# Optimization experiments

Hardware: AMD Instinct MI355X
Metric: run time of the kernel (lower is better)

Reference implementation:

```python
import jax, jax.numpy as jnp
import numpy as np

B, S, I, H = 256, 512, 512, 1024


def setup_inputs() -> dict:
    key = jax.random.key(0)
    ks = jax.random.split(key, 7)
    s = 1.0 / np.sqrt(H)
    x = jax.random.normal(ks[0], (B, S, I), jnp.float32)
    # equinox GRUCell params: weight_ih (3H,I), weight_hh (3H,H), bias (3H,), bias_n (H,)
    wi = jax.random.uniform(ks[1], (3 * H, I), jnp.float32, -s, s)
    wh = jax.random.uniform(ks[2], (3 * H, H), jnp.float32, -s, s)
    bi = jax.random.uniform(ks[3], (3 * H,), jnp.float32, -s, s)
    bn = jax.random.uniform(ks[4], (H,), jnp.float32, -s, s)
    # final Linear(H, 1)
    sl = 1.0 / np.sqrt(H)
    wl = jax.random.uniform(ks[5], (1, H), jnp.float32, -sl, sl)
    bl = jax.random.uniform(ks[6], (1,), jnp.float32, -sl, sl)
    return {"x": x, "wi": wi, "wh": wh, "bi": bi, "bn": bn, "wl": wl, "bl": bl}


def reference(x, wi, wh, bi, bn, wl, bl):
    # x: (B, S, I). Precompute input-side gate projections for all timesteps
    # (same math as per-step wi @ x_t + bi, hoisted out of the scan).
    ig_all = jnp.einsum('bsi,gi->sbg', x, wi) + bi  # (S, B, 3H)

    def step(h, ig_t):
        hg = h @ wh.T  # (B, 3H)
        ir, iz, ia = jnp.split(ig_t, 3, axis=-1)
        hr, hz, ha = jnp.split(hg, 3, axis=-1)
        r = jax.nn.sigmoid(ir + hr)          # reset gate
        z = jax.nn.sigmoid(iz + hz)          # update gate (equinox 'inp')
        n = jnp.tanh(ia + r * (ha + bn))     # candidate (uses bias_n)
        h_new = n + z * (h - n)              # equinox GRUCell output
        return h_new, None

    h0 = jnp.zeros((x.shape[0], wh.shape[1]), x.dtype)
    hT, _ = jax.lax.scan(step, h0, ig_all)
    energies = hT @ wl.T + bl  # (B, 1)
    return jnp.squeeze(energies, axis=-1)  # (B,)
```

## Files before the change

### kernel.cpp

```cpp
#include <hip/hip_runtime.h>
#include <hip/hip_bf16.h>


#define B_  256
#define S_  512
#define I_  512
#define H_  1024

typedef __bf16 bf16x8 __attribute__((ext_vector_type(8)));
typedef float  f32x4  __attribute__((ext_vector_type(4)));
typedef float  f32x4v __attribute__((ext_vector_type(4)));

union U16x8 { int4 i; bf16x8 b; unsigned short s[8]; unsigned u[4]; };

__device__ __forceinline__ unsigned pack2bf(float lo, float hi) {
    union { float f; unsigned u; } a, b;
    a.f = lo; b.f = hi;
    return __builtin_amdgcn_perm(b.u + 0x8000u, a.u + 0x8000u, 0x07060302u);
}
__device__ __forceinline__ bf16x8 ldb(const unsigned short* p) {
    U16x8 u; u.i = *(const int4*)p; return u.b;
}
__device__ __forceinline__ bf16x8 ldh_dev(const unsigned long long* p) {
    unsigned long long lo = __hip_atomic_load(p,     __ATOMIC_RELAXED, __HIP_MEMORY_SCOPE_AGENT);
    unsigned long long hi = __hip_atomic_load(p + 1, __ATOMIC_RELAXED, __HIP_MEMORY_SCOPE_AGENT);
    union { unsigned long long q[2]; bf16x8 b; } u;
    u.q[0] = lo; u.q[1] = hi; return u.b;
}

__global__ void prep_kernel(const float* __restrict__ wh, const float* __restrict__ wi,
                            const float* __restrict__ x,
                            unsigned* __restrict__ hbA_u, unsigned* __restrict__ whb_u,
                            unsigned* __restrict__ wib_u, unsigned* __restrict__ flags,
                            unsigned* __restrict__ xb_u, unsigned* __restrict__ xw_u,
                            int W) {
    int idx = blockIdx.x * blockDim.x + threadIdx.x;
    int stride = gridDim.x * blockDim.x;
    const float2* wh2 = (const float2*)wh;
    const float2* wi2 = (const float2*)wi;
    for (int i = idx; i < 3 * H_ * H_ / 2; i += stride) { float2 v = wh2[i]; whb_u[i] = pack2bf(v.x, v.y); }
    for (int i = idx; i < 3 * H_ * I_ / 2; i += stride) { float2 v = wi2[i]; wib_u[i] = pack2bf(v.x, v.y); }
    for (int i = idx; i < B_ * H_ / 2; i += stride) hbA_u[i] = 0u;
    if (idx < 256 * 4 * 16) flags[idx] = 0u;
    if (xb_u) {
        const float2* x2 = (const float2*)x;
        const int n = B_ * S_ * I_ / 2;
        for (int i = idx; i < n; i += stride) { float2 v = x2[i]; xb_u[i] = pack2bf(v.x, v.y); }
    }
    if (xw_u) {
        const int total = 4 * W * 16384;
        for (int i = idx; i < total; i += stride) {
            int gslot = i >> 14;
            int rest  = i & 16383;
            int row   = rest >> 8;
            int cp    = rest & 255;
            int mt    = gslot / W;
            int s     = gslot - mt * W;
            const float2 v = *(const float2*)(x + ((size_t)(mt * 64 + row) * S_ + s) * I_ + (cp << 1));
            xw_u[i] = pack2bf(v.x, v.y);
        }
    }
}

template<int MODE>
__global__ __launch_bounds__(256, 1) void gru_persistent(
    const float* __restrict__ x,
    const unsigned short* __restrict__ xbp,
    unsigned* __restrict__ xww,
    const unsigned short* __restrict__ whb,
    const unsigned short* __restrict__ wib,
    const float* __restrict__ bi,
    const float* __restrict__ bn,
    unsigned short* __restrict__ hbufA,
    unsigned short* __restrict__ hbufB,
    float* __restrict__ h32g,
    unsigned* __restrict__ flags,
    int wmask)
{
    __shared__ float partial[4 * 3 * 16 * 68];
    __shared__ float h32s[64 * 17];

    const int tid  = threadIdx.x;
    const int w    = tid >> 6;
    const int lane = tid & 63;
    const int col  = lane & 15;
    const int quad = lane >> 4;

    const int hblk = blockIdx.x & 63;
    const int mt   = blockIdx.x >> 6;
    const int k0   = hblk << 4;
    const int b0   = mt << 6;
    const int kwh  = w << 8;
    const int kwi  = w << 7;

    bf16x8 Bh[3][8];
    bf16x8 Bx[3][4];
    #pragma unroll
    for (int g = 0; g < 3; ++g) {
        const unsigned short* bh = whb + ((size_t)(g * H_ + k0 + col)) * H_ + kwh + (quad << 3);
        #pragma unroll
        for (int kk = 0; kk < 8; ++kk) Bh[g][kk] = ldb(bh + kk * 32);
        const unsigned short* bx = wib + ((size_t)(g * H_ + k0 + col)) * I_ + kwi + (quad << 3);
        #pragma unroll
        for (int kk = 0; kk < 4; ++kk) Bx[g][kk] = ldb(bx + kk * 32);
    }

    const int hcol = k0 + col;
    const float bir = bi[hcol], biz = bi[H_ + hcol], bia = bi[2 * H_ + hcol], bnv = bn[hcol];

    for (int i = tid; i < 64 * 17; i += 256) h32s[i] = 0.f;
    __syncthreads();

    unsigned* myflag = flags + (((blockIdx.x << 2) + w) << 4);
    const unsigned* spin_fp = flags +
        ((((mt << 6) + (w << 4) + (lane >> 2)) * 4 + (lane & 3)) << 4);

    const f32x4 zero4 = {0.f, 0.f, 0.f, 0.f};

    for (int t = 0; t < S_; ++t) {
        f32x4 acc[4][4];
        #pragma unroll
        for (int mi = 0; mi < 4; ++mi)
            #pragma unroll
            for (int j = 0; j < 4; ++j) acc[mi][j] = zero4;

        bool early_ok = true;
        if (t > 0)
            early_ok = (__hip_atomic_load(spin_fp, __ATOMIC_RELAXED, __HIP_MEMORY_SCOPE_AGENT) >= (unsigned)t);

        if constexpr (MODE == 2) {
            const unsigned short* xbase = xbp + ((size_t)(b0 + col) * S_ + (size_t)t) * I_ + kwi + (quad << 3);
            #pragma unroll
            for (int kk = 0; kk < 4; ++kk) {
                #pragma unroll
                for (int mi = 0; mi < 4; ++mi) {
                    bf16x8 a = ldb(xbase + (size_t)mi * 16 * S_ * I_ + kk * 32);
                    acc[mi][0] = __builtin_amdgcn_mfma_f32_16x16x32_bf16(a, Bx[0][kk], acc[mi][0], 0, 0, 0);
                    acc[mi][1] = __builtin_amdgcn_mfma_f32_16x16x32_bf16(a, Bx[1][kk], acc[mi][1], 0, 0, 0);
                    acc[mi][2] = __builtin_amdgcn_mfma_f32_16x16x32_bf16(a, Bx[2][kk], acc[mi][2], 0, 0, 0);
                }
            }
        } else if constexpr (MODE == 1) {
            const int W = wmask + 1;
            const unsigned short* xbase = xbp
                + ((size_t)((mt * W + (t & wmask)) * 64 + col)) * I_ + kwi + (quad << 3);
            #pragma unroll
            for (int kk = 0; kk < 4; ++kk) {
                #pragma unroll
                for (int mi = 0; mi < 4; ++mi) {
                    bf16x8 a = ldh_dev((const unsigned long long*)(xbase + (size_t)mi * 16 * I_ + kk * 32));
                    acc[mi][0] = __builtin_amdgcn_mfma_f32_16x16x32_bf16(a, Bx[0][kk], acc[mi][0], 0, 0, 0);
                    acc[mi][1] = __builtin_amdgcn_mfma_f32_16x16x32_bf16(a, Bx[1][kk], acc[mi][1], 0, 0, 0);
                    acc[mi][2] = __builtin_amdgcn_mfma_f32_16x16x32_bf16(a, Bx[2][kk], acc[mi][2], 0, 0, 0);
                }
            }
        } else {
            const float* xbase = x + ((size_t)(b0 + col) * S_ + (size_t)t) * I_ + kwi + (quad << 3);
            #pragma unroll
            for (int kk = 0; kk < 4; ++kk) {
                #pragma unroll
                for (int mi = 0; mi < 4; ++mi) {
                    const float* p = xbase + (size_t)mi * 16 * S_ * I_ + kk * 32;
                    f32x4v f0 = __builtin_nontemporal_load((const f32x4v*)p);
                    f32x4v f1 = __builtin_nontemporal_load((const f32x4v*)(p + 4));
                    U16x8 u;
                    u.u[0] = pack2bf(f0[0], f0[1]);
                    u.u[1] = pack2bf(f0[2], f0[3]);
                    u.u[2] = pack2bf(f1[0], f1[1]);
                    u.u[3] = pack2bf(f1[2], f1[3]);
                    bf16x8 a = u.b;
                    acc[mi][0] = __builtin_amdgcn_mfma_f32_16x16x32_bf16(a, Bx[0][kk], acc[mi][0], 0, 0, 0);
                    acc[mi][1] = __builtin_amdgcn_mfma_f32_16x16x32_bf16(a, Bx[1][kk], acc[mi][1], 0, 0, 0);
                    acc[mi][2] = __builtin_amdgcn_mfma_f32_16x16x32_bf16(a, Bx[2][kk], acc[mi][2], 0, 0, 0);
                }
            }
        }

        if (t > 0) {
            if (!early_ok) {
                while (__hip_atomic_load(spin_fp, __ATOMIC_RELAXED, __HIP_MEMORY_SCOPE_AGENT) < (unsigned)t)
                    __builtin_amdgcn_s_sleep(1);
            }
            asm volatile("" ::: "memory");
        }

        const unsigned short* hcur = (t & 1) ? hbufB : hbufA;
        const unsigned short* hrow = hcur + (size_t)(b0 + col) * H_ + kwh + (quad << 3);
        {
            bf16x8 hf[2][4];
            #pragma unroll
            for (int mi = 0; mi < 4; ++mi)
                hf[0][mi] = ldh_dev((const unsigned long long*)(hrow + (size_t)mi * 16 * H_));
            #pragma unroll
            for (int kk = 0; kk < 8; ++kk) {
                if (kk < 7) {
                    #pragma unroll
                    for (int mi = 0; mi < 4; ++mi)
                        hf[(kk + 1) & 1][mi] = ldh_dev((const unsigned long long*)(hrow + (size_t)mi * 16 * H_ + (kk + 1) * 32));
                }
                #pragma unroll
                for (int mi = 0; mi < 4; ++mi) {
                    bf16x8 a = hf[kk & 1][mi];
                    acc[mi][0] = __builtin_amdgcn_mfma_f32_16x16x32_bf16(a, Bh[0][kk], acc[mi][0], 0, 0, 0);
                    acc[mi][1] = __builtin_amdgcn_mfma_f32_16x16x32_bf16(a, Bh[1][kk], acc[mi][1], 0, 0, 0);
                    acc[mi][3] = __builtin_amdgcn_mfma_f32_16x16x32_bf16(a, Bh[2][kk], acc[mi][3], 0, 0, 0);
                }
            }
        }

        if constexpr (MODE == 1) {
            const int W = wmask + 1;
            const int s = t + W - 1;
            if (t >= 1 && s < S_) {
                const int flat = (hblk << 8) + tid;
                const int row  = flat >> 8;
                const int cp   = flat & 255;
                const float2 v = *(const float2*)(x + ((size_t)(b0 + row) * S_ + s) * I_ + (cp << 1));
                const unsigned pkt = pack2bf(v.x, v.y);
                __hip_atomic_store(xww + ((size_t)((mt * W + (s & wmask))) << 14) + flat,
                                   pkt, __ATOMIC_RELAXED, __HIP_MEMORY_SCOPE_AGENT);
            }
        }

        #pragma unroll
        for (int mi = 0; mi < 4; ++mi) {
            if (mi == w) continue;
            int slot = mi - (mi > w ? 1 : 0);
            float* dst = partial + (size_t)((w * 3 + slot) * 16) * 68;
            #pragma unroll
            for (int j = 0; j < 4; ++j)
                #pragma unroll
                for (int r = 0; r < 4; ++r)
                    dst[((quad << 2) + r) * 68 + j * 16 + col] = acc[mi][j][r];
        }
        __syncthreads();

        #pragma unroll
        for (int r = 0; r < 4; ++r) {
            float sr = 0.f, sz = 0.f, sia = 0.f, sha = 0.f;
            #pragma unroll
            for (int mi = 0; mi < 4; ++mi)
                if (mi == w) { sr = acc[mi][0][r]; sz = acc[mi][1][r]; sia = acc[mi][2][r]; sha = acc[mi][3][r]; }
            #pragma unroll
            for (int p = 0; p < 4; ++p) {
                if (p == w) continue;
                int slot = w - (w > p ? 1 : 0);
                const float* src = partial + (size_t)(((p * 3 + slot) * 16 + (quad << 2) + r)) * 68 + col;
                sr  += src[0];
                sz  += src[16];
                sia += src[32];
                sha += src[48];
            }
            float rg = 1.f / (1.f + __expf(-(sr + bir)));
            float zg = 1.f / (1.f + __expf(-(sz + biz)));
            float pa = sia + bia + rg * (sha + bnv);
            float e2 = __expf(2.f * pa);
            float ng = 1.f - 2.f / (e2 + 1.f);
            int m = (w << 4) + (quad << 2) + r;
            float hold = h32s[m * 17 + col];
            float hnew = ng + zg * (hold - ng);
            h32s[m * 17 + col] = hnew;
            if (t == S_ - 1) h32g[(size_t)(b0 + m) * H_ + k0 + col] = hnew;
        }
        __syncthreads();

        {
            unsigned short* hnext = (t & 1) ? hbufA : hbufB;
            const int pm = (w << 4) + (lane >> 2);
            const int pc = (lane & 3) << 2;
            const float* hp = h32s + pm * 17 + pc;
            unsigned long long pkt = (unsigned long long)pack2bf(hp[0], hp[1])
                                   | ((unsigned long long)pack2bf(hp[2], hp[3]) << 32);
            __hip_atomic_store((unsigned long long*)(hnext + (size_t)(b0 + pm) * H_ + k0 + pc),
                               pkt, __ATOMIC_RELAXED, __HIP_MEMORY_SCOPE_AGENT);
            asm volatile("s_waitcnt vmcnt(0)" ::: "memory");
            if (lane == 0)
                __hip_atomic_store(myflag, (unsigned)(t + 1), __ATOMIC_RELAXED, __HIP_MEMORY_SCOPE_AGENT);
        }
    }
}

__global__ __launch_bounds__(256) void final_kernel(const float* __restrict__ h32,
                                                    const float* __restrict__ wl,
                                                    const float* __restrict__ bl,
                                                    float* __restrict__ out) {
    const int b = blockIdx.x;
    float s = 0.f;
    for (int k = threadIdx.x; k < H_; k += 256)
        s += h32[((size_t)b << 10) + k] * wl[k];
    #pragma unroll
    for (int off = 32; off > 0; off >>= 1)
        s += __shfl_down(s, off, 64);
    __shared__ float red[4];
    const int wave = threadIdx.x >> 6;
    const int lane = threadIdx.x & 63;
    if (lane == 0) red[wave] = s;
    __syncthreads();
    if (threadIdx.x == 0)
        out[b] = red[0] + red[1] + red[2] + red[3] + bl[0];
}

extern "C" void kernel_launch(void* const* d_in, const int* in_sizes, int n_in,
                              void* d_out, int out_size, void* d_ws, size_t ws_size,
                              hipStream_t stream) {
    const float* x  = (const float*)d_in[0];
    const float* wi = (const float*)d_in[1];
    const float* wh = (const float*)d_in[2];
    const float* bi = (const float*)d_in[3];
    const float* bn = (const float*)d_in[4];
    const float* wl = (const float*)d_in[5];
    const float* bl = (const float*)d_in[6];
    float* out = (float*)d_out;

    char* ws = (char*)d_ws;
    float*          h32g  = (float*)ws;
    unsigned short* hbA   = (unsigned short*)(ws + (1u << 20));
    unsigned short* hbB   = (unsigned short*)(ws + (1u << 20) + (512u << 10));
    unsigned short* whb   = (unsigned short*)(ws + (2u << 20));
    unsigned short* wib   = (unsigned short*)(ws + (8u << 20));
    unsigned*       flags = (unsigned*)(ws + (11u << 20));

    unsigned short* xbw = nullptr;
    unsigned*       xww = nullptr;
    int W = 0;
    if (ws_size >= (141ull << 20)) {
        xbw = (unsigned short*)(ws + (12ull << 20));
    } else if (ws_size >= (13ull << 20)) {
        size_t avail = ws_size - (12ull << 20);
        W = 4;
        while (W < 64 && ((size_t)(W * 2) << 18) <= avail) W <<= 1;
        xww = (unsigned*)(ws + (12ull << 20));
    }

    prep_kernel<<<1024, 256, 0, stream>>>(wh, wi, x, (unsigned*)hbA, (unsigned*)whb,
                                          (unsigned*)wib, flags, (unsigned*)xbw, xww, W);
    if (xbw)
        gru_persistent<2><<<256, 256, 0, stream>>>(x, xbw, nullptr, whb, wib, bi, bn,
                                                   hbA, hbB, h32g, flags, 0);
    else if (xww)
        gru_persistent<1><<<256, 256, 0, stream>>>(x, (const unsigned short*)xww, xww, whb, wib, bi, bn,
                                                   hbA, hbB, h32g, flags, W - 1);
    else
        gru_persistent<0><<<256, 256, 0, stream>>>(x, nullptr, nullptr, whb, wib, bi, bn,
                                                   hbA, hbB, h32g, flags, 0);
    final_kernel<<<B_, 256, 0, stream>>>(h32g, wl, bl, out);
}
```

Baseline: 8.220 ms.

## Fuse final linear into GRU kernel and restructure x-window ring buffer

Removes the separate final_kernel: prep initializes out with the bias, and the last timestep reduces hnew*wl across lanes and atomically adds into out. The MODE 1 x-conversion ring is resized to non-power-of-two W using a rotating slot index, the next x slice is loaded early and stored after the step's barrier, and the workspace is repacked so more staging fits. MODE 0 switches from nontemporal to plain loads. The atomicAdd reduction makes the output summation order nondeterministic.

New measurement: 8.293 ms. Within noise of the previous version (+0.9%).

```diff
diff --git a/kernel.cpp b/kernel.cpp
--- a/kernel.cpp
+++ b/kernel.cpp
@@ -9,7 +9,7 @@
 
 typedef __bf16 bf16x8 __attribute__((ext_vector_type(8)));
 typedef float  f32x4  __attribute__((ext_vector_type(4)));
-typedef float  f32x4v __attribute__((ext_vector_type(4)));
+typedef float  f32x2v __attribute__((ext_vector_type(2)));
 
 union U16x8 { int4 i; bf16x8 b; unsigned short s[8]; unsigned u[4]; };
 
@@ -29,9 +29,10 @@
 }
 
 __global__ void prep_kernel(const float* __restrict__ wh, const float* __restrict__ wi,
-                            const float* __restrict__ x,
+                            const float* __restrict__ x,  const float* __restrict__ bl,
                             unsigned* __restrict__ hbA_u, unsigned* __restrict__ whb_u,
                             unsigned* __restrict__ wib_u, unsigned* __restrict__ flags,
+                            float* __restrict__ out,
                             unsigned* __restrict__ xb_u, unsigned* __restrict__ xw_u,
                             int W) {
     int idx = blockIdx.x * blockDim.x + threadIdx.x;
@@ -42,6 +43,7 @@
     for (int i = idx; i < 3 * H_ * I_ / 2; i += stride) { float2 v = wi2[i]; wib_u[i] = pack2bf(v.x, v.y); }
     for (int i = idx; i < B_ * H_ / 2; i += stride) hbA_u[i] = 0u;
     if (idx < 256 * 4 * 16) flags[idx] = 0u;
+    if (idx < B_) out[idx] = bl[0];
     if (xb_u) {
         const float2* x2 = (const float2*)x;
         const int n = B_ * S_ * I_ / 2;
@@ -71,11 +73,12 @@
     const unsigned short* __restrict__ wib,
     const float* __restrict__ bi,
     const float* __restrict__ bn,
+    const float* __restrict__ wl,
     unsigned short* __restrict__ hbufA,
     unsigned short* __restrict__ hbufB,
-    float* __restrict__ h32g,
+    float* __restrict__ out,
     unsigned* __restrict__ flags,
-    int wmask)
+    int W)
 {
     __shared__ float partial[4 * 3 * 16 * 68];
     __shared__ float h32s[64 * 17];
@@ -107,6 +110,7 @@
 
     const int hcol = k0 + col;
     const float bir = bi[hcol], biz = bi[H_ + hcol], bia = bi[2 * H_ + hcol], bnv = bn[hcol];
+    const float wlv = wl[hcol];
 
     for (int i = tid; i < 64 * 17; i += 256) h32s[i] = 0.f;
     __syncthreads();
@@ -117,12 +121,28 @@
 
     const f32x4 zero4 = {0.f, 0.f, 0.f, 0.f};
 
+    int slot_rd = 0;
+
     for (int t = 0; t < S_; ++t) {
         f32x4 acc[4][4];
         #pragma unroll
         for (int mi = 0; mi < 4; ++mi)
             #pragma unroll
             for (int j = 0; j < 4; ++j) acc[mi][j] = zero4;
+
+        float cvx = 0.f, cvy = 0.f;
+        int   swr = 0;
+        bool  do_conv = false;
+        if constexpr (MODE == 1) {
+            const int s = t + W - 1;
+            if (t >= 1 && s < S_) {
+                do_conv = true;
+                f32x2v c = __builtin_nontemporal_load(
+                    (const f32x2v*)(x + ((size_t)(b0 + hblk) * S_ + s) * I_ + (tid << 1)));
+                cvx = c[0]; cvy = c[1];
+                swr = (slot_rd == 0) ? (W - 1) : (slot_rd - 1);
+            }
+        }
 
         bool early_ok = true;
         if (t > 0)
@@ -141,9 +161,8 @@
                 }
             }
         } else if constexpr (MODE == 1) {
-            const int W = wmask + 1;
             const unsigned short* xbase = xbp
-                + ((size_t)((mt * W + (t & wmask)) * 64 + col)) * I_ + kwi + (quad << 3);
+                + ((size_t)((mt * W + slot_rd) * 64 + col)) * I_ + kwi + (quad << 3);
             #pragma unroll
             for (int kk = 0; kk < 4; ++kk) {
                 #pragma unroll
@@ -161,13 +180,13 @@
                 #pragma unroll
                 for (int mi = 0; mi < 4; ++mi) {
                     const float* p = xbase + (size_t)mi * 16 * S_ * I_ + kk * 32;
-                    f32x4v f0 = __builtin_nontemporal_load((const f32x4v*)p);
-                    f32x4v f1 = __builtin_nontemporal_load((const f32x4v*)(p + 4));
+                    float4 f0 = *(const float4*)p;
+                    float4 f1 = *(const float4*)(p + 4);
                     U16x8 u;
-                    u.u[0] = pack2bf(f0[0], f0[1]);
-                    u.u[1] = pack2bf(f0[2], f0[3]);
-                    u.u[2] = pack2bf(f1[0], f1[1]);
-                    u.u[3] = pack2bf(f1[2], f1[3]);
+                    u.u[0] = pack2bf(f0.x, f0.y);
+                    u.u[1] = pack2bf(f0.z, f0.w);
+                    u.u[2] = pack2bf(f1.x, f1.y);
+                    u.u[3] = pack2bf(f1.z, f1.w);
                     bf16x8 a = u.b;
                     acc[mi][0] = __builtin_amdgcn_mfma_f32_16x16x32_bf16(a, Bx[0][kk], acc[mi][0], 0, 0, 0);
                     acc[mi][1] = __builtin_amdgcn_mfma_f32_16x16x32_bf16(a, Bx[1][kk], acc[mi][1], 0, 0, 0);
@@ -205,20 +224,6 @@
                     acc[mi][1] = __builtin_amdgcn_mfma_f32_16x16x32_bf16(a, Bh[1][kk], acc[mi][1], 0, 0, 0);
                     acc[mi][3] = __builtin_amdgcn_mfma_f32_16x16x32_bf16(a, Bh[2][kk], acc[mi][3], 0, 0, 0);
                 }
-            }
-        }
-
-        if constexpr (MODE == 1) {
-            const int W = wmask + 1;
-            const int s = t + W - 1;
-            if (t >= 1 && s < S_) {
-                const int flat = (hblk << 8) + tid;
-                const int row  = flat >> 8;
-                const int cp   = flat & 255;
-                const float2 v = *(const float2*)(x + ((size_t)(b0 + row) * S_ + s) * I_ + (cp << 1));
-                const unsigned pkt = pack2bf(v.x, v.y);
-                __hip_atomic_store(xww + ((size_t)((mt * W + (s & wmask))) << 14) + flat,
-                                   pkt, __ATOMIC_RELAXED, __HIP_MEMORY_SCOPE_AGENT);
             }
         }
 
@@ -260,10 +265,22 @@
             float hold = h32s[m * 17 + col];
             float hnew = ng + zg * (hold - ng);
             h32s[m * 17 + col] = hnew;
-            if (t == S_ - 1) h32g[(size_t)(b0 + m) * H_ + k0 + col] = hnew;
+            if (t == S_ - 1) {
+                float e = hnew * wlv;
+                e += __shfl_xor(e, 1, 16);
+                e += __shfl_xor(e, 2, 16);
+                e += __shfl_xor(e, 4, 16);
+                e += __shfl_xor(e, 8, 16);
+                if (col == 0) atomicAdd(out + b0 + m, e);
+            }
         }
         __syncthreads();
 
+        if constexpr (MODE == 1) {
+            if (do_conv)
+                __hip_atomic_store(xww + ((size_t)(mt * W + swr) << 14) + (hblk << 8) + tid,
+                                   pack2bf(cvx, cvy), __ATOMIC_RELAXED, __HIP_MEMORY_SCOPE_AGENT);
+        }
         {
             unsigned short* hnext = (t & 1) ? hbufA : hbufB;
             const int pm = (w << 4) + (lane >> 2);
@@ -277,27 +294,10 @@
             if (lane == 0)
                 __hip_atomic_store(myflag, (unsigned)(t + 1), __ATOMIC_RELAXED, __HIP_MEMORY_SCOPE_AGENT);
         }
-    }
-}
-
-__global__ __launch_bounds__(256) void final_kernel(const float* __restrict__ h32,
-                                                    const float* __restrict__ wl,
-                                                    const float* __restrict__ bl,
-                                                    float* __restrict__ out) {
-    const int b = blockIdx.x;
-    float s = 0.f;
-    for (int k = threadIdx.x; k < H_; k += 256)
-        s += h32[((size_t)b << 10) + k] * wl[k];
-    #pragma unroll
-    for (int off = 32; off > 0; off >>= 1)
-        s += __shfl_down(s, off, 64);
-    __shared__ float red[4];
-    const int wave = threadIdx.x >> 6;
-    const int lane = threadIdx.x & 63;
-    if (lane == 0) red[wave] = s;
-    __syncthreads();
-    if (threadIdx.x == 0)
-        out[b] = red[0] + red[1] + red[2] + red[3] + bl[0];
+
+        if constexpr (MODE == 1)
+            slot_rd = (slot_rd + 1 == W) ? 0 : slot_rd + 1;
+    }
 }
 
 extern "C" void kernel_launch(void* const* d_in, const int* in_sizes, int n_in,
@@ -313,35 +313,35 @@
     float* out = (float*)d_out;
 
     char* ws = (char*)d_ws;
-    float*          h32g  = (float*)ws;
-    unsigned short* hbA   = (unsigned short*)(ws + (1u << 20));
-    unsigned short* hbB   = (unsigned short*)(ws + (1u << 20) + (512u << 10));
-    unsigned short* whb   = (unsigned short*)(ws + (2u << 20));
-    unsigned short* wib   = (unsigned short*)(ws + (8u << 20));
-    unsigned*       flags = (unsigned*)(ws + (11u << 20));
+    unsigned short* whb   = (unsigned short*)ws;
+    unsigned short* wib   = (unsigned short*)(ws + (6ull << 20));
+    unsigned short* hbA   = (unsigned short*)(ws + (9ull << 20));
+    unsigned short* hbB   = (unsigned short*)(ws + (9ull << 20) + (512ull << 10));
+    unsigned*       flags = (unsigned*)(ws + (10ull << 20));
+    char*           xbase = ws + (10ull << 20) + (64ull << 10);
+    const size_t    base  = (10ull << 20) + (64ull << 10);
 
     unsigned short* xbw = nullptr;
     unsigned*       xww = nullptr;
     int W = 0;
-    if (ws_size >= (141ull << 20)) {
-        xbw = (unsigned short*)(ws + (12ull << 20));
-    } else if (ws_size >= (13ull << 20)) {
-        size_t avail = ws_size - (12ull << 20);
-        W = 4;
-        while (W < 64 && ((size_t)(W * 2) << 18) <= avail) W <<= 1;
-        xww = (unsigned*)(ws + (12ull << 20));
-    }
-
-    prep_kernel<<<1024, 256, 0, stream>>>(wh, wi, x, (unsigned*)hbA, (unsigned*)whb,
-                                          (unsigned*)wib, flags, (unsigned*)xbw, xww, W);
+    if (ws_size >= base + (128ull << 20)) {
+        xbw = (unsigned short*)xbase;
+    } else if (ws_size >= base + 3ull * 262144ull) {
+        size_t avail = ws_size - base;
+        size_t wmax  = avail / 262144ull;
+        W = (int)(wmax > 64 ? 64 : wmax);
+        xww = (unsigned*)xbase;
+    }
+
+    prep_kernel<<<1024, 256, 0, stream>>>(wh, wi, x, bl, (unsigned*)hbA, (unsigned*)whb,
+                                          (unsigned*)wib, flags, out, (unsigned*)xbw, xww, W);
     if (xbw)
-        gru_persistent<2><<<256, 256, 0, stream>>>(x, xbw, nullptr, whb, wib, bi, bn,
-                                                   hbA, hbB, h32g, flags, 0);
+        gru_persistent<2><<<256, 256, 0, stream>>>(x, xbw, nullptr, whb, wib, bi, bn, wl,
+                                                   hbA, hbB, out, flags, 0);
     else if (xww)
-        gru_persistent<1><<<256, 256, 0, stream>>>(x, (const unsigned short*)xww, xww, whb, wib, bi, bn,
-                                                   hbA, hbB, h32g, flags, W - 1);
+        gru_persistent<1><<<256, 256, 0, stream>>>(x, (const unsigned short*)xww, xww, whb, wib, bi, bn, wl,
+                                                   hbA, hbB, out, flags, W);
     else
-        gru_persistent<0><<<256, 256, 0, stream>>>(x, nullptr, nullptr, whb, wib, bi, bn,
-                                                   hbA, hbB, h32g, flags, 0);
-    final_kernel<<<B_, 256, 0, stream>>>(h32g, wl, bl, out);
-}
+        gru_persistent<0><<<256, 256, 0, stream>>>(x, nullptr, nullptr, whb, wib, bi, bn, wl,
+                                                   hbA, hbB, out, flags, 0);
+}
```
